# Kernel tuning notes

Hardware: AMD Instinct MI355X
Metric: run time of the kernel (lower is better)

Reference implementation:

```python
import jax, jax.numpy as jnp
import numpy as np

B, D, S = 16, 64, 2048


def setup_inputs() -> dict:
    key = jax.random.key(0)
    kq, kk, kv, km = jax.random.split(key, 4)
    q = jax.random.normal(kq, (B, D, S), dtype=jnp.float32)
    k = jax.random.normal(kk, (B, D, S), dtype=jnp.float32)
    v = jax.random.normal(kv, (B, D, S), dtype=jnp.float32)
    # boolean mask over the [B, Sq, Sk] score matrix (True -> filled with -1000)
    mask = jax.random.bernoulli(km, 0.1, (B, S, S))
    return {"q": q, "k": k, "v": v, "mask": mask}


def reference(q, k, v, mask):
    dim = jnp.asarray(D, dtype=q.dtype)
    # scores[b, s, t] = sum_d q[b, d, s] * k[b, d, t] / sqrt(D)
    scores = jnp.einsum("bds,bdt->bst", q, k) / jnp.sqrt(dim)
    scores = jnp.where(mask, jnp.asarray(-1000.0, dtype=scores.dtype), scores)
    # NOTE: softmax over dim=1 (the QUERY axis), faithful to nn.Softmax(dim=1)
    attn = jax.nn.softmax(scores, axis=1)
    # out[b, s, d] = sum_t attn[b, s, t] * v[b, d, t]
    out = jnp.einsum("bst,bdt->bsd", attn, v)
    return out
```

## Files before the change

kernel.cpp:

```cpp
#include <hip/hip_runtime.h>
#include <hip/hip_bf16.h>
#include <stdint.h>


namespace {
constexpr int B = 16;
constexpr int D = 64;
constexpr int S = 2048;
constexpr float SCALE = 0.125f;

typedef __attribute__((ext_vector_type(8))) short short8;
typedef __attribute__((ext_vector_type(4))) float f32x4;

constexpr size_t WS_FLAG  = 0;
constexpr size_t WS_LINV  = 256;
constexpr size_t WS_LPART = 256 + 131072;
constexpr size_t WS_QT    = WS_LPART + 4194304;
constexpr size_t WS_KT    = WS_QT + 4194304;
constexpr size_t WS_VB    = WS_KT + 4194304;
constexpr size_t WS_MPACK = WS_VB + 4194304;
constexpr size_t NEED_NEW = WS_MPACK + 8388608;
}

__device__ __forceinline__ bool mask_at(const void* mask, int mode, size_t idx) {
    if (mode == 1) return ((const int*)mask)[idx] != 0;
    if (mode == 2) return ((const float*)mask)[idx] != 0.0f;
    return ((const unsigned char*)mask)[idx] != 0;
}

__device__ __forceinline__ uint16_t f2bf(float f) {
    unsigned int u = __float_as_uint(f);
    unsigned int r = (u + 0x7fffu + ((u >> 16) & 1u)) >> 16;
    return (uint16_t)r;
}
__device__ __forceinline__ unsigned int pack2(float a, float b) {
    return (unsigned int)f2bf(a) | ((unsigned int)f2bf(b) << 16);
}

__device__ __forceinline__ int swz(int row, int colByte) {
    return row * 128 + (colByte ^ ((row & 7) << 4));
}

__device__ __forceinline__ void gll16(const void* g, void* l) {
    __builtin_amdgcn_global_load_lds(
        (const __attribute__((address_space(1))) void*)g,
        (__attribute__((address_space(3))) void*)l, 16, 0, 0);
}

__device__ __forceinline__ void stage_tile(const char* srcRows, size_t rowStrideB,
                                           unsigned char* dst, int tid) {
    const int lane = tid & 63, w = tid >> 6;
    const int lrow = lane >> 3;
    const int slot = (lane & 7) ^ lrow;
    #pragma unroll
    for (int c = 0; c < 2; ++c) {
        const int row = 16 * w + 8 * c + lrow;
        gll16(srcRows + (size_t)row * rowStrideB + slot * 16,
              dst + (16 * w + 8 * c) * 128);
    }
}

__device__ __forceinline__ void stage_tile32(const char* srcRows, size_t rowStrideB,
                                             unsigned char* dst, int tid) {
    const int lane = tid & 63, w = tid >> 6;
    const int lrow = lane >> 3;
    const int slot = (lane & 7) ^ lrow;
    const int row = 8 * w + lrow;
    gll16(srcRows + (size_t)row * rowStrideB + slot * 16, dst + 8 * w * 128);
}

__device__ __forceinline__ f32x4 mfma16(short8 a, short8 b, f32x4 c) {
    return __builtin_amdgcn_mfma_f32_16x16x32_bf16(a, b, c, 0, 0, 0);
}

__device__ __forceinline__ void probe_body(const unsigned char* mask, int* flag,
                                           int tid, int* c0s, int* c123s) {
    if (tid == 0) { *c0s = 0; *c123s = 0; }
    __syncthreads();
    int c0 = 0, c123 = 0;
    for (int f = tid; f < 65536; f += 256) {
        const int nz = (mask[f] != 0) ? 1 : 0;
        if ((f & 3) == 0) c0 += nz; else c123 += nz;
    }
    atomicAdd(c0s, c0);
    atomicAdd(c123s, c123);
    __syncthreads();
    if (tid == 0) {
        int mode = 0;
        if (*c123s == 0) mode = 1;
        else if (*c0s == 0) mode = 2;
        *flag = mode;
    }
}

__global__ void probe_mask_kernel(const unsigned char* __restrict__ mask,
                                  int* __restrict__ flag)
{
    __shared__ int c0s, c123s;
    probe_body(mask, flag, threadIdx.x, &c0s, &c123s);
}

__global__ __launch_bounds__(256, 2)
void prep_kernel(const float* __restrict__ q, const float* __restrict__ k,
                 const float* __restrict__ v,
                 uint16_t* __restrict__ qT, uint16_t* __restrict__ kT,
                 uint16_t* __restrict__ vb,
                 const unsigned char* __restrict__ mask, int* __restrict__ flag)
{
    __shared__ float ts[64][65];
    const int tid = threadIdx.x;
    const int s0 = blockIdx.x * 64;
    const int b  = blockIdx.y;

    if (blockIdx.z == 2) {
        const int d = tid >> 2, c = tid & 3;
        const float* row = v + ((size_t)b * D + d) * S + s0 + c * 16;
        uint16_t*   orow = vb + ((size_t)b * D + d) * S + s0 + c * 16;
        #pragma unroll
        for (int i = 0; i < 4; ++i) {
            float4 v4 = *(const float4*)(row + 4 * i);
            uint16_t t4[4] = {f2bf(v4.x), f2bf(v4.y), f2bf(v4.z), f2bf(v4.w)};
            *(uint2*)(orow + 4 * i) = *(const uint2*)t4;
        }
        if (blockIdx.x == 0 && blockIdx.y == 0) {
            __shared__ int c0s, c123s;
            probe_body(mask, flag, tid, &c0s, &c123s);
        }
        return;
    }

    const float* src = blockIdx.z ? k : q;
    uint16_t*    dst = blockIdx.z ? kT : qT;
    {
        const int d = tid >> 2, c = tid & 3;
        const float* row = src + ((size_t)b * D + d) * S + s0 + c * 16;
        #pragma unroll
        for (int i = 0; i < 4; ++i) {
            float4 v4 = *(const float4*)(row + 4 * i);
            ts[c * 16 + 4 * i + 0][d] = v4.x;
            ts[c * 16 + 4 * i + 1][d] = v4.y;
            ts[c * 16 + 4 * i + 2][d] = v4.z;
            ts[c * 16 + 4 * i + 3][d] = v4.w;
        }
    }
    __syncthreads();
    {
        const int srow = tid >> 2, p = tid & 3;
        uint16_t tmp[16];
        #pragma unroll
        for (int j = 0; j < 16; ++j) tmp[j] = f2bf(ts[srow][p * 16 + j]);
        uint16_t* drow = dst + ((size_t)b * S + s0 + srow) * 64 + p * 16;
        *(uint4*)drow       = ((const uint4*)tmp)[0];
        *((uint4*)drow + 1) = ((const uint4*)tmp)[1];
    }
}

__global__ __launch_bounds__(256, 4)
void pass1_kernel(const uint16_t* __restrict__ qT, const uint16_t* __restrict__ kT,
                  const void* __restrict__ mask, const int* __restrict__ flagp,
                  float* __restrict__ lpart, unsigned long long* __restrict__ mpackT)
{
    __shared__ __align__(16) unsigned char qsb[64 * 128];
    __shared__ __align__(16) unsigned char ksb[2][64 * 128];
    __shared__ unsigned short mbits[64][4];
    __shared__ float red[2][4][64];

    const int tid = threadIdx.x;
    const int lane = tid & 63, w = tid >> 6;
    const int l = lane & 15, hh = lane >> 4;
    const int sb = blockIdx.x;
    const int th = blockIdx.y;
    const int b  = blockIdx.z;
    const int s0 = sb * 64;
    const int tbase = th * 1024;
    const int mode = *flagp;
    const bool wide = (mode != 0);

    const int row_m = tid >> 2, cq = tid & 3;
    const size_t mrow = ((size_t)b * S + s0 + row_m) * S + tbase + cq * 16;

    int4  mr4[4];
    uint4 mr1;
    auto load_mtile = [&](int tt) {
        if (wide) {
            const int4* p = (const int4*)((const int*)mask + mrow + tt * 64);
            mr4[0] = p[0]; mr4[1] = p[1]; mr4[2] = p[2]; mr4[3] = p[3];
        } else {
            mr1 = *(const uint4*)((const unsigned char*)mask + mrow + tt * 64);
        }
    };
    auto pack_mtile = [&]() -> unsigned int {
        unsigned int bits = 0;
        if (wide) {
            #pragma unroll
            for (int i = 0; i < 4; ++i) {
                bits |= (mr4[i].x ? 1u : 0u) << (4 * i + 0);
                bits |= (mr4[i].y ? 1u : 0u) << (4 * i + 1);
                bits |= (mr4[i].z ? 1u : 0u) << (4 * i + 2);
                bits |= (mr4[i].w ? 1u : 0u) << (4 * i + 3);
            }
        } else {
            const unsigned int u[4] = {mr1.x, mr1.y, mr1.z, mr1.w};
            #pragma unroll
            for (int c = 0; c < 4; ++c) {
                bits |= ((u[c] & 0x000000FFu) ? 1u : 0u) << (4 * c + 0);
                bits |= ((u[c] & 0x0000FF00u) ? 1u : 0u) << (4 * c + 1);
                bits |= ((u[c] & 0x00FF0000u) ? 1u : 0u) << (4 * c + 2);
                bits |= ((u[c] & 0xFF000000u) ? 1u : 0u) << (4 * c + 3);
            }
        }
        return bits;
    };

    stage_tile((const char*)(qT + ((size_t)b * S + s0) * 64), 128, qsb, tid);
    stage_tile((const char*)(kT + ((size_t)b * S + tbase) * 64), 128, ksb[0], tid);
    load_mtile(0);
    __syncthreads();

    const short8 A0 = *(const short8*)&qsb[swz(16 * w + l, 0  + hh * 16)];
    const short8 A1 = *(const short8*)&qsb[swz(16 * w + l, 64 + hh * 16)];

    const int srow_l = 16 * w + 4 * hh;
    const size_t mpk_b = (size_t)b * 32 + th * 16;
    const size_t lp_base = ((size_t)b * 32 + sb) * S + tbase;

    for (int tt = 0; tt < 16; ++tt) {
        const int cur = tt & 1;

        __syncthreads();

        if (tt > 0 && tid < 64) {
            const int p = cur ^ 1;
            lpart[lp_base + (size_t)(tt - 1) * 64 + tid] =
                red[p][0][tid] + red[p][1][tid] + red[p][2][tid] + red[p][3][tid];
        }

        const unsigned int bits = pack_mtile();
        mbits[row_m][cq] = (unsigned short)bits;

        if (tt < 15) {
            stage_tile((const char*)(kT + ((size_t)b * S + tbase + (tt + 1) * 64) * 64),
                       128, ksb[cur ^ 1], tid);
            load_mtile(tt + 1);
        }

        if (lane < 16) {
            const int rr = 16 * w + lane;
            const unsigned long long word =
                (unsigned long long)mbits[rr][0]
                | ((unsigned long long)mbits[rr][1] << 16)
                | ((unsigned long long)mbits[rr][2] << 32)
                | ((unsigned long long)mbits[rr][3] << 48);
            mpackT[(mpk_b + tt) * S + s0 + rr] = word;
        }

        float colacc[4] = {0.f, 0.f, 0.f, 0.f};
        #pragma unroll
        for (int tf = 0; tf < 4; ++tf) {
            const short8 B0 = *(const short8*)&ksb[cur][swz(tf * 16 + l, 0  + hh * 16)];
            const short8 B1 = *(const short8*)&ksb[cur][swz(tf * 16 + l, 64 + hh * 16)];
            f32x4 c4 = {0.f, 0.f, 0.f, 0.f};
            c4 = mfma16(A0, B0, c4);
            c4 = mfma16(A1, B1, c4);
            #pragma unroll
            for (int r = 0; r < 4; ++r) {
                if (!((mbits[srow_l + r][tf] >> l) & 1))
                    colacc[tf] += __expf(c4[r] * SCALE);
            }
        }

        #pragma unroll
        for (int tf = 0; tf < 4; ++tf) {
            colacc[tf] += __shfl_xor(colacc[tf], 16);
            colacc[tf] += __shfl_xor(colacc[tf], 32);
        }
        if (lane < 16) {
            #pragma unroll
            for (int tf = 0; tf < 4; ++tf) red[cur][w][tf * 16 + lane] = colacc[tf];
        }
    }

    __syncthreads();
    if (tid < 64) {
        lpart[lp_base + (size_t)15 * 64 + tid] =
            red[1][0][tid] + red[1][1][tid] + red[1][2][tid] + red[1][3][tid];
    }
}

__global__ void linv_kernel(const float* __restrict__ lpart, float* __restrict__ linv)
{
    const int i = blockIdx.x * 256 + threadIdx.x;
    const int b = i >> 11, t = i & (S - 1);
    float s = 0.f;
    #pragma unroll 8
    for (int sb = 0; sb < 32; ++sb)
        s += lpart[((size_t)b * 32 + sb) * S + t];
    linv[i] = 1.0f / s;
}

__global__ __launch_bounds__(256, 4)
void pass2_kernel(const uint16_t* __restrict__ qT, const uint16_t* __restrict__ kT,
                  const uint16_t* __restrict__ vb,
                  const unsigned long long* __restrict__ mpackT,
                  const float* __restrict__ linv, float* __restrict__ out)
{
    __shared__ __align__(16) unsigned char qsb[32 * 128];
    __shared__ __align__(16) unsigned char ksb[64 * 128];
    __shared__ __align__(16) unsigned char vsb[64 * 128];
    __shared__ __align__(16) unsigned char ptb[32 * 128];
    __shared__ unsigned long long mrow2[2][32];
    __shared__ float linv_s[2][64];

    const int tid = threadIdx.x;
    const int lane = tid & 63, w = tid >> 6;
    const int l = lane & 15, hh = lane >> 4;
    const int s0 = blockIdx.x * 32;
    const int b = blockIdx.y;

    auto load_meta = [&](int tile, int slot) {
        if (tid < 64) {
            linv_s[slot][tid] = linv[(size_t)b * S + tile * 64 + tid];
        } else if (tid < 96) {
            mrow2[slot][tid - 64] =
                mpackT[((size_t)b * 32 + tile) * S + s0 + (tid - 64)];
        }
    };

    stage_tile32((const char*)(qT + ((size_t)b * S + s0) * 64), 128, qsb, tid);
    stage_tile((const char*)(kT + (size_t)b * S * 64), 128, ksb, tid);
    stage_tile((const char*)(vb + (size_t)b * D * S), (size_t)S * 2, vsb, tid);
    load_meta(0, 0);
    __syncthreads();

    short8 QB[2][2];
    #pragma unroll
    for (int sf = 0; sf < 2; ++sf)
        #pragma unroll
        for (int kh = 0; kh < 2; ++kh)
            QB[sf][kh] = *(const short8*)&qsb[swz(sf * 16 + l, kh * 64 + hh * 16)];

    f32x4 oacc[2];
    oacc[0] = (f32x4){0.f, 0.f, 0.f, 0.f};
    oacc[1] = (f32x4){0.f, 0.f, 0.f, 0.f};

    const int sbd = w & 1;
    const int dh = w >> 1;

    for (int i = 0; i < 32; ++i) {
        const int cur = i & 1, nxt = cur ^ 1;

        if (i > 0)
            stage_tile((const char*)(vb + (size_t)b * D * S + i * 64),
                       (size_t)S * 2, vsb, tid);

        short8 KA0 = *(const short8*)&ksb[swz(16 * w + l, 0  + hh * 16)];
        short8 KA1 = *(const short8*)&ksb[swz(16 * w + l, 64 + hh * 16)];
        float lv[4];
        #pragma unroll
        for (int r = 0; r < 4; ++r) lv[r] = linv_s[cur][16 * w + 4 * hh + r];

        #pragma unroll
        for (int sf = 0; sf < 2; ++sf) {
            f32x4 c4 = {0.f, 0.f, 0.f, 0.f};
            c4 = mfma16(KA0, QB[sf][0], c4);
            c4 = mfma16(KA1, QB[sf][1], c4);
            const unsigned long long bits = mrow2[cur][sf * 16 + l];
            float pv[4];
            #pragma unroll
            for (int r = 0; r < 4; ++r) {
                const int tloc = 16 * w + 4 * hh + r;
                pv[r] = ((bits >> tloc) & 1ull) ? 0.f : __expf(c4[r] * SCALE) * lv[r];
            }
            const int row = sf * 16 + l;
            const int cb = (32 * w + 8 * hh);
            *(uint2*)&ptb[row * 128 + (cb ^ ((row & 7) << 4))] =
                make_uint2(pack2(pv[0], pv[1]), pack2(pv[2], pv[3]));
        }
        __syncthreads();

        if (i + 1 < 32) {
            stage_tile((const char*)(kT + ((size_t)b * S + (i + 1) * 64) * 64),
                       128, ksb, tid);
            load_meta(i + 1, nxt);
        }

        short8 PA0 = *(const short8*)&ptb[swz(sbd * 16 + l, 0  + hh * 16)];
        short8 PA1 = *(const short8*)&ptb[swz(sbd * 16 + l, 64 + hh * 16)];
        #pragma unroll
        for (int df = 0; df < 2; ++df) {
            const int drow = (dh * 2 + df) * 16 + l;
            short8 VB0 = *(const short8*)&vsb[swz(drow, 0  + hh * 16)];
            short8 VB1 = *(const short8*)&vsb[swz(drow, 64 + hh * 16)];
            oacc[df] = mfma16(PA0, VB0, oacc[df]);
            oacc[df] = mfma16(PA1, VB1, oacc[df]);
        }
        __syncthreads();
    }

    #pragma unroll
    for (int df = 0; df < 2; ++df)
        #pragma unroll
        for (int r = 0; r < 4; ++r)
            out[((size_t)b * S + s0 + sbd * 16 + 4 * hh + r) * D
                + (dh * 2 + df) * 16 + l] = oacc[df][r];
}

__global__ __launch_bounds__(256, 2)
void colsum_fb(const float* __restrict__ q, const float* __restrict__ k,
               const void* __restrict__ mask, const int* __restrict__ flagp,
               float* __restrict__ lsums)
{
    __shared__ __align__(16) float qs[128][68];
    __shared__ __align__(16) float ks[64][68];
    __shared__ float lred[32][66];
    const int tid = threadIdx.x;
    const int b = blockIdx.y;
    const int t0 = blockIdx.x * 64;
    const int mode = *flagp;
    {
        const int tl = tid & 63, d0 = tid >> 6;
        #pragma unroll
        for (int i = 0; i < 16; ++i) { const int d = d0 + i * 4; ks[tl][d] = k[(b * D + d) * S + t0 + tl]; }
    }
    const int tq = tid & 7, sq = tid >> 3;
    float lacc[8];
    #pragma unroll
    for (int j = 0; j < 8; ++j) lacc[j] = 0.f;
    const size_t mbase = (size_t)b * S * S;
    for (int s0 = 0; s0 < S; s0 += 128) {
        __syncthreads();
        {
            const int sl = tid & 127, d0 = tid >> 7;
            #pragma unroll
            for (int i = 0; i < 32; ++i) { const int d = d0 + i * 2; qs[sl][d] = q[(b * D + d) * S + s0 + sl]; }
        }
        __syncthreads();
        float acc[4][8];
        #pragma unroll
        for (int jj = 0; jj < 4; ++jj)
            #pragma unroll
            for (int j = 0; j < 8; ++j) acc[jj][j] = 0.f;
        #pragma unroll
        for (int dblk = 0; dblk < 16; ++dblk) {
            float4 q4[4];
            #pragma unroll
            for (int jj = 0; jj < 4; ++jj) q4[jj] = *(const float4*)&qs[sq + 32 * jj][dblk * 4];
            #pragma unroll
            for (int j = 0; j < 8; ++j) {
                const float4 k4 = *(const float4*)&ks[tq + 8 * j][dblk * 4];
                #pragma unroll
                for (int jj = 0; jj < 4; ++jj)
                    acc[jj][j] += q4[jj].x * k4.x + q4[jj].y * k4.y + q4[jj].z * k4.z + q4[jj].w * k4.w;
            }
        }
        #pragma unroll
        for (int jj = 0; jj < 4; ++jj) {
            const int sg = s0 + sq + 32 * jj;
            const size_t ridx = mbase + (size_t)sg * S + t0;
            #pragma unroll
            for (int j = 0; j < 8; ++j)
                if (!mask_at(mask, mode, ridx + tq + 8 * j)) lacc[j] += __expf(acc[jj][j] * SCALE);
        }
    }
    __syncthreads();
    #pragma unroll
    for (int j = 0; j < 8; ++j) lred[sq][tq + 8 * j] = lacc[j];
    __syncthreads();
    if (tid < 64) {
        float s = 0.f;
        #pragma unroll
        for (int i = 0; i < 32; ++i) s += lred[i][tid];
        lsums[b * S + t0 + tid] = s;
    }
}

__global__ __launch_bounds__(256, 2)
void attn_out_fb(const float* __restrict__ q, const float* __restrict__ k,
                 const float* __restrict__ v, const void* __restrict__ mask,
                 const int* __restrict__ flagp, const float* __restrict__ lsums,
                 float* __restrict__ out)
{
    __shared__ __align__(16) float qs[64][68];
    __shared__ __align__(16) float kw[64][68];
    __shared__ __align__(16) float pt[64][68];
    __shared__ float linv_sh[64];
    const int tid = threadIdx.x;
    const int b = blockIdx.y;
    const int s0 = blockIdx.x * 64;
    const int mode = *flagp;
    {
        const int sl = tid & 63, d0 = tid >> 6;
        #pragma unroll
        for (int i = 0; i < 16; ++i) { const int d = d0 + i * 4; qs[sl][d] = q[(b * D + d) * S + s0 + sl]; }
    }
    const int tq = tid & 7, sq = tid >> 3;
    float oacc[2][8];
    #pragma unroll
    for (int jj = 0; jj < 2; ++jj)
        #pragma unroll
        for (int dd = 0; dd < 8; ++dd) oacc[jj][dd] = 0.f;
    const size_t mbase = (size_t)b * S * S;
    for (int t0 = 0; t0 < S; t0 += 64) {
        __syncthreads();
        if (tid < 64) linv_sh[tid] = 1.f / lsums[b * S + t0 + tid];
        {
            const int tl = tid & 63, d0 = tid >> 6;
            #pragma unroll
            for (int i = 0; i < 16; ++i) { const int d = d0 + i * 4; kw[tl][d] = k[(b * D + d) * S + t0 + tl]; }
        }
        __syncthreads();
        float sc[2][8];
        #pragma unroll
        for (int jj = 0; jj < 2; ++jj)
            #pragma unroll
            for (int j = 0; j < 8; ++j) sc[jj][j] = 0.f;
        #pragma unroll
        for (int dblk = 0; dblk < 16; ++dblk) {
            float4 q4[2];
            #pragma unroll
            for (int jj = 0; jj < 2; ++jj) q4[jj] = *(const float4*)&qs[sq + 32 * jj][dblk * 4];
            #pragma unroll
            for (int j = 0; j < 8; ++j) {
                const float4 k4 = *(const float4*)&kw[tq + 8 * j][dblk * 4];
                #pragma unroll
                for (int jj = 0; jj < 2; ++jj)
                    sc[jj][j] += q4[jj].x * k4.x + q4[jj].y * k4.y + q4[jj].z * k4.z + q4[jj].w * k4.w;
            }
        }
        #pragma unroll
        for (int jj = 0; jj < 2; ++jj) {
            const int sg = s0 + sq + 32 * jj;
            const size_t ridx = mbase + (size_t)sg * S + t0;
            #pragma unroll
            for (int j = 0; j < 8; ++j) {
                const int tl = tq + 8 * j;
                const bool msk = mask_at(mask, mode, ridx + tl);
                pt[tl][sq + 32 * jj] = msk ? 0.f : __expf(sc[jj][j] * SCALE) * linv_sh[tl];
            }
        }
        __syncthreads();
        {
            const int tl = tid & 63, d0 = tid >> 6;
            #pragma unroll
            for (int i = 0; i < 16; ++i) { const int d = d0 + i * 4; kw[tl][d] = v[(b * D + d) * S + t0 + tl]; }
        }
        __syncthreads();
        #pragma unroll 8
        for (int t = 0; t < 64; ++t) {
            const float2 p2 = *(const float2*)&pt[t][sq * 2];
            const float4 w0 = *(const float4*)&kw[t][tq * 8];
            const float4 w1 = *(const float4*)&kw[t][tq * 8 + 4];
            oacc[0][0] += p2.x * w0.x; oacc[0][1] += p2.x * w0.y; oacc[0][2] += p2.x * w0.z; oacc[0][3] += p2.x * w0.w;
            oacc[0][4] += p2.x * w1.x; oacc[0][5] += p2.x * w1.y; oacc[0][6] += p2.x * w1.z; oacc[0][7] += p2.x * w1.w;
            oacc[1][0] += p2.y * w0.x; oacc[1][1] += p2.y * w0.y; oacc[1][2] += p2.y * w0.z; oacc[1][3] += p2.y * w0.w;
            oacc[1][4] += p2.y * w1.x; oacc[1][5] += p2.y * w1.y; oacc[1][6] += p2.y * w1.z; oacc[1][7] += p2.y * w1.w;
        }
    }
    #pragma unroll
    for (int jj = 0; jj < 2; ++jj) {
        float* dst = out + ((size_t)(b * S + s0 + sq * 2 + jj)) * D + tq * 8;
        *(float4*)dst = make_float4(oacc[jj][0], oacc[jj][1], oacc[jj][2], oacc[jj][3]);
        *(float4*)(dst + 4) = make_float4(oacc[jj][4], oacc[jj][5], oacc[jj][6], oacc[jj][7]);
    }
}

extern "C" void kernel_launch(void* const* d_in, const int* in_sizes, int n_in,
                              void* d_out, int out_size, void* d_ws, size_t ws_size,
                              hipStream_t stream) {
    const float* q = (const float*)d_in[0];
    const float* k = (const float*)d_in[1];
    const float* v = (const float*)d_in[2];
    const void*  mask = d_in[3];
    float* out = (float*)d_out;
    char* ws = (char*)d_ws;

    int* flag = (int*)(ws + WS_FLAG);

    if (ws_size >= NEED_NEW) {
        float*    linv  = (float*)(ws + WS_LINV);
        float*    lpart = (float*)(ws + WS_LPART);
        uint16_t* qT    = (uint16_t*)(ws + WS_QT);
        uint16_t* kT    = (uint16_t*)(ws + WS_KT);
        uint16_t* vb    = (uint16_t*)(ws + WS_VB);
        unsigned long long* mpackT = (unsigned long long*)(ws + WS_MPACK);

        prep_kernel<<<dim3(S / 64, B, 3), 256, 0, stream>>>(
            q, k, v, qT, kT, vb, (const unsigned char*)mask, flag);
        pass1_kernel<<<dim3(32, 2, B), 256, 0, stream>>>(
            qT, kT, mask, flag, lpart, mpackT);
        linv_kernel<<<(B * S) / 256, 256, 0, stream>>>(lpart, linv);
        pass2_kernel<<<dim3(S / 32, B), 256, 0, stream>>>(
            qT, kT, vb, mpackT, linv, out);
    } else {
        float* lsums = (float*)(ws + WS_LINV);
        probe_mask_kernel<<<1, 256, 0, stream>>>((const unsigned char*)mask, flag);
        dim3 grid(S / 64, B);
        colsum_fb<<<grid, 256, 0, stream>>>(q, k, mask, flag, lsums);
        attn_out_fb<<<grid, 256, 0, stream>>>(q, k, v, mask, flag, lsums, out);
    }
}
```

Baseline: 178.7 us.

## Move mask bit-packing from pass1 into prep kernel, feed pass1 prepacked bits

The mask-to-bitmask packing moves out of pass1 into extra blocks of the prep kernel, which read whole mask rows and write the transposed packed words. Pass1 then loads 64-bit packed mask words instead of streaming the raw mask, which shrinks its memory traffic and register pressure. The mode probe now runs as a separate single-block kernel before prep, adding one serial launch. The first loop-top barrier in pass1 is also skipped.

```diff
diff --git a/kernel.cpp b/kernel.cpp
--- a/kernel.cpp
+++ b/kernel.cpp
@@ -73,45 +73,100 @@
     return __builtin_amdgcn_mfma_f32_16x16x32_bf16(a, b, c, 0, 0, 0);
 }
 
-__device__ __forceinline__ void probe_body(const unsigned char* mask, int* flag,
-                                           int tid, int* c0s, int* c123s) {
-    if (tid == 0) { *c0s = 0; *c123s = 0; }
+__global__ void probe_mask_kernel(const unsigned char* __restrict__ mask,
+                                  int* __restrict__ flag)
+{
+    __shared__ int c0s, c123s;
+    const int tid = threadIdx.x;
+    if (tid == 0) { c0s = 0; c123s = 0; }
     __syncthreads();
     int c0 = 0, c123 = 0;
     for (int f = tid; f < 65536; f += 256) {
         const int nz = (mask[f] != 0) ? 1 : 0;
         if ((f & 3) == 0) c0 += nz; else c123 += nz;
     }
-    atomicAdd(c0s, c0);
-    atomicAdd(c123s, c123);
+    atomicAdd(&c0s, c0);
+    atomicAdd(&c123s, c123);
     __syncthreads();
     if (tid == 0) {
         int mode = 0;
-        if (*c123s == 0) mode = 1;
-        else if (*c0s == 0) mode = 2;
+        if (c123s == 0) mode = 1;
+        else if (c0s == 0) mode = 2;
         *flag = mode;
     }
 }
 
-__global__ void probe_mask_kernel(const unsigned char* __restrict__ mask,
-                                  int* __restrict__ flag)
+__global__ __launch_bounds__(256, 2)
+void prep_mpack_kernel(const float* __restrict__ q, const float* __restrict__ k,
+                       const float* __restrict__ v,
+                       uint16_t* __restrict__ qT, uint16_t* __restrict__ kT,
+                       uint16_t* __restrict__ vb,
+                       const void* __restrict__ mask, const int* __restrict__ flagp,
+                       unsigned long long* __restrict__ mpackT)
 {
-    __shared__ int c0s, c123s;
-    probe_body(mask, flag, threadIdx.x, &c0s, &c123s);
-}
-
-__global__ __launch_bounds__(256, 2)
-void prep_kernel(const float* __restrict__ q, const float* __restrict__ k,
-                 const float* __restrict__ v,
-                 uint16_t* __restrict__ qT, uint16_t* __restrict__ kT,
-                 uint16_t* __restrict__ vb,
-                 const unsigned char* __restrict__ mask, int* __restrict__ flag)
-{
-    __shared__ float ts[64][65];
+    __shared__ __align__(16) unsigned char shmem[16704];
     const int tid = threadIdx.x;
+    const int b = blockIdx.y;
+
+    if (blockIdx.z >= 3) {
+        unsigned int (*warr)[130] = (unsigned int(*)[130])shmem;
+        const int sblk = blockIdx.x + (blockIdx.z - 3) * 32;
+        const int s0 = sblk * 32;
+        const int mode = *flagp;
+        const int lane = tid & 63, w = tid >> 6;
+        const int t64 = lane >> 1, half = lane & 1;
+
+        #pragma unroll 2
+        for (int rr = 0; rr < 8; ++rr) {
+            const int sl = w * 8 + rr;
+            unsigned int bits = 0;
+            if (mode != 0) {
+                const int4* rowv = (const int4*)((const int*)mask +
+                                   ((size_t)b * S + s0 + sl) * S);
+                #pragma unroll
+                for (int i = 0; i < 8; ++i) {
+                    const int4 v4 = rowv[lane * 8 + i];
+                    bits |= (v4.x ? 1u : 0u) << (4 * i + 0);
+                    bits |= (v4.y ? 1u : 0u) << (4 * i + 1);
+                    bits |= (v4.z ? 1u : 0u) << (4 * i + 2);
+                    bits |= (v4.w ? 1u : 0u) << (4 * i + 3);
+                }
+            } else {
+                const uint4* rowv = (const uint4*)((const unsigned char*)mask +
+                                    ((size_t)b * S + s0 + sl) * S);
+                #pragma unroll
+                for (int i = 0; i < 2; ++i) {
+                    const uint4 v4 = rowv[lane * 2 + i];
+                    const unsigned int u4[4] = {v4.x, v4.y, v4.z, v4.w};
+                    #pragma unroll
+                    for (int c = 0; c < 4; ++c) {
+                        const unsigned int u = u4[c];
+                        const int base = 16 * i + 4 * c;
+                        bits |= ((u & 0x000000FFu) ? 1u : 0u) << (base + 0);
+                        bits |= ((u & 0x0000FF00u) ? 1u : 0u) << (base + 1);
+                        bits |= ((u & 0x00FF0000u) ? 1u : 0u) << (base + 2);
+                        bits |= ((u & 0xFF000000u) ? 1u : 0u) << (base + 3);
+                    }
+                }
+            }
+            warr[t64][sl * 2 + half] = bits;
+        }
+        __syncthreads();
+
+        #pragma unroll
+        for (int i = 0; i < 4; ++i) {
+            const int idx = i * 256 + tid;
+            const int ot = idx >> 5;
+            const int os = idx & 31;
+            const unsigned long long word =
+                (unsigned long long)warr[ot][os * 2] |
+                ((unsigned long long)warr[ot][os * 2 + 1] << 32);
+            mpackT[((size_t)b * 32 + ot) * S + s0 + os] = word;
+        }
+        return;
+    }
+
     const int s0 = blockIdx.x * 64;
-    const int b  = blockIdx.y;
-
     if (blockIdx.z == 2) {
         const int d = tid >> 2, c = tid & 3;
         const float* row = v + ((size_t)b * D + d) * S + s0 + c * 16;
@@ -122,13 +177,10 @@
             uint16_t t4[4] = {f2bf(v4.x), f2bf(v4.y), f2bf(v4.z), f2bf(v4.w)};
             *(uint2*)(orow + 4 * i) = *(const uint2*)t4;
         }
-        if (blockIdx.x == 0 && blockIdx.y == 0) {
-            __shared__ int c0s, c123s;
-            probe_body(mask, flag, tid, &c0s, &c123s);
-        }
         return;
     }
 
+    float (*ts)[65] = (float(*)[65])shmem;
     const float* src = blockIdx.z ? k : q;
     uint16_t*    dst = blockIdx.z ? kT : qT;
     {
@@ -157,12 +209,12 @@
 
 __global__ __launch_bounds__(256, 4)
 void pass1_kernel(const uint16_t* __restrict__ qT, const uint16_t* __restrict__ kT,
-                  const void* __restrict__ mask, const int* __restrict__ flagp,
-                  float* __restrict__ lpart, unsigned long long* __restrict__ mpackT)
+                  const unsigned long long* __restrict__ mpackT,
+                  float* __restrict__ lpart)
 {
     __shared__ __align__(16) unsigned char qsb[64 * 128];
     __shared__ __align__(16) unsigned char ksb[2][64 * 128];
-    __shared__ unsigned short mbits[64][4];
+    __shared__ unsigned long long mrow[2][64];
     __shared__ float red[2][4][64];
 
     const int tid = threadIdx.x;
@@ -173,61 +225,23 @@
     const int b  = blockIdx.z;
     const int s0 = sb * 64;
     const int tbase = th * 1024;
-    const int mode = *flagp;
-    const bool wide = (mode != 0);
-
-    const int row_m = tid >> 2, cq = tid & 3;
-    const size_t mrow = ((size_t)b * S + s0 + row_m) * S + tbase + cq * 16;
-
-    int4  mr4[4];
-    uint4 mr1;
-    auto load_mtile = [&](int tt) {
-        if (wide) {
-            const int4* p = (const int4*)((const int*)mask + mrow + tt * 64);
-            mr4[0] = p[0]; mr4[1] = p[1]; mr4[2] = p[2]; mr4[3] = p[3];
-        } else {
-            mr1 = *(const uint4*)((const unsigned char*)mask + mrow + tt * 64);
-        }
-    };
-    auto pack_mtile = [&]() -> unsigned int {
-        unsigned int bits = 0;
-        if (wide) {
-            #pragma unroll
-            for (int i = 0; i < 4; ++i) {
-                bits |= (mr4[i].x ? 1u : 0u) << (4 * i + 0);
-                bits |= (mr4[i].y ? 1u : 0u) << (4 * i + 1);
-                bits |= (mr4[i].z ? 1u : 0u) << (4 * i + 2);
-                bits |= (mr4[i].w ? 1u : 0u) << (4 * i + 3);
-            }
-        } else {
-            const unsigned int u[4] = {mr1.x, mr1.y, mr1.z, mr1.w};
-            #pragma unroll
-            for (int c = 0; c < 4; ++c) {
-                bits |= ((u[c] & 0x000000FFu) ? 1u : 0u) << (4 * c + 0);
-                bits |= ((u[c] & 0x0000FF00u) ? 1u : 0u) << (4 * c + 1);
-                bits |= ((u[c] & 0x00FF0000u) ? 1u : 0u) << (4 * c + 2);
-                bits |= ((u[c] & 0xFF000000u) ? 1u : 0u) << (4 * c + 3);
-            }
-        }
-        return bits;
-    };
+
+    const size_t mpk_b = (size_t)b * 32 + th * 16;
+    const size_t lp_base = ((size_t)b * 32 + sb) * S + tbase;
 
     stage_tile((const char*)(qT + ((size_t)b * S + s0) * 64), 128, qsb, tid);
     stage_tile((const char*)(kT + ((size_t)b * S + tbase) * 64), 128, ksb[0], tid);
-    load_mtile(0);
+    if (tid < 64) mrow[0][tid] = mpackT[mpk_b * S + s0 + tid];
     __syncthreads();
 
     const short8 A0 = *(const short8*)&qsb[swz(16 * w + l, 0  + hh * 16)];
     const short8 A1 = *(const short8*)&qsb[swz(16 * w + l, 64 + hh * 16)];
-
     const int srow_l = 16 * w + 4 * hh;
-    const size_t mpk_b = (size_t)b * 32 + th * 16;
-    const size_t lp_base = ((size_t)b * 32 + sb) * S + tbase;
 
     for (int tt = 0; tt < 16; ++tt) {
         const int cur = tt & 1;
 
-        __syncthreads();
+        if (tt > 0) __syncthreads();
 
         if (tt > 0 && tid < 64) {
             const int p = cur ^ 1;
@@ -235,23 +249,10 @@
                 red[p][0][tid] + red[p][1][tid] + red[p][2][tid] + red[p][3][tid];
         }
 
-        const unsigned int bits = pack_mtile();
-        mbits[row_m][cq] = (unsigned short)bits;
-
         if (tt < 15) {
             stage_tile((const char*)(kT + ((size_t)b * S + tbase + (tt + 1) * 64) * 64),
                        128, ksb[cur ^ 1], tid);
-            load_mtile(tt + 1);
-        }
-
-        if (lane < 16) {
-            const int rr = 16 * w + lane;
-            const unsigned long long word =
-                (unsigned long long)mbits[rr][0]
-                | ((unsigned long long)mbits[rr][1] << 16)
-                | ((unsigned long long)mbits[rr][2] << 32)
-                | ((unsigned long long)mbits[rr][3] << 48);
-            mpackT[(mpk_b + tt) * S + s0 + rr] = word;
+            if (tid < 64) mrow[cur ^ 1][tid] = mpackT[(mpk_b + tt + 1) * S + s0 + tid];
         }
 
         float colacc[4] = {0.f, 0.f, 0.f, 0.f};
@@ -264,7 +265,7 @@
             c4 = mfma16(A1, B1, c4);
             #pragma unroll
             for (int r = 0; r < 4; ++r) {
-                if (!((mbits[srow_l + r][tf] >> l) & 1))
+                if (!((mrow[cur][srow_l + r] >> (tf * 16 + l)) & 1ull))
                     colacc[tf] += __expf(c4[r] * SCALE);
             }
         }
@@ -584,10 +585,10 @@
         uint16_t* vb    = (uint16_t*)(ws + WS_VB);
         unsigned long long* mpackT = (unsigned long long*)(ws + WS_MPACK);
 
-        prep_kernel<<<dim3(S / 64, B, 3), 256, 0, stream>>>(
-            q, k, v, qT, kT, vb, (const unsigned char*)mask, flag);
-        pass1_kernel<<<dim3(32, 2, B), 256, 0, stream>>>(
-            qT, kT, mask, flag, lpart, mpackT);
+        probe_mask_kernel<<<1, 256, 0, stream>>>((const unsigned char*)mask, flag);
+        prep_mpack_kernel<<<dim3(32, B, 5), 256, 0, stream>>>(
+            q, k, v, qT, kT, vb, mask, flag, mpackT);
+        pass1_kernel<<<dim3(32, 2, B), 256, 0, stream>>>(qT, kT, mpackT, lpart);
         linv_kernel<<<(B * S) / 256, 256, 0, stream>>>(lpart, linv);
         pass2_kernel<<<dim3(S / 32, B), 256, 0, stream>>>(
             qT, kT, vb, mpackT, linv, out);
```

New measurement: 198.3 us. +11.0%, slower.
